# Kernel optimization log

Hardware: AMD Instinct MI355X
Metric: run time of the kernel (lower is better)

## Reference

```python
import jax, jax.numpy as jnp
import numpy as np

H = 12      # num_attention_heads
DM = 768    # hidden_size
HD = DM // H  # head_dim = 64


def setup_inputs() -> dict:
    key = jax.random.key(0)
    ks = jax.random.split(key, 9)
    B, L = 4, 2048
    s = 0.02
    return {
        "hidden_states": jax.random.normal(ks[0], (B, L, DM), jnp.float32),
        "wq": jax.random.normal(ks[1], (DM, DM), jnp.float32) * s,
        "bq": jnp.zeros((DM,), jnp.float32),
        "wk": jax.random.normal(ks[2], (DM, DM), jnp.float32) * s,
        "bk": jnp.zeros((DM,), jnp.float32),
        "wv": jax.random.normal(ks[3], (DM, DM), jnp.float32) * s,
        "bv": jnp.zeros((DM,), jnp.float32),
        "wo": jax.random.normal(ks[4], (DM, DM), jnp.float32) * s,
        "bo": jnp.zeros((DM,), jnp.float32),
    }


def reference(hidden_states, wq, bq, wk, bk, wv, bv, wo, bo):
    B, L, D = hidden_states.shape
    scale = HD ** -0.5
    # torch Linear: x @ W.T + b
    q = hidden_states @ wq.T + bq
    k = hidden_states @ wk.T + bk
    v = hidden_states @ wv.T + bv
    # [B, H, L, HD]
    q = q.reshape(B, L, H, HD).transpose(0, 2, 1, 3)
    k = k.reshape(B, L, H, HD).transpose(0, 2, 1, 3)
    v = v.reshape(B, L, H, HD).transpose(0, 2, 1, 3)
    attn = jnp.einsum('bhqd,bhkd->bhqk', q, k) * scale
    causal = jnp.tril(jnp.ones((L, L), dtype=bool))
    attn = jnp.where(causal, attn, jnp.float32(-jnp.inf))
    attn = jax.nn.softmax(attn, axis=-1)
    out = jnp.einsum('bhqk,bhkd->bhqd', attn, v)
    out = out.transpose(0, 2, 1, 3).reshape(B, L, D)
    return out @ wo.T + bo
```

## Files before the change

### kernel.cpp

```cpp
#include <hip/hip_runtime.h>

typedef unsigned short ushort_t;
typedef __attribute__((ext_vector_type(8))) short short8;
typedef __attribute__((ext_vector_type(4))) float f32x4;

__device__ __forceinline__ ushort_t f2b(float f) {
    union { float f; unsigned int i; } v; v.f = f;
    unsigned int x = v.i;
    return (ushort_t)((x + 0x7fffu + ((x >> 16) & 1u)) >> 16);
}
__device__ __forceinline__ ushort_t f2b_fast(float f) {
    union { float f; unsigned int i; } v; v.f = f;
    return (ushort_t)((v.i + 0x8000u) >> 16);
}
__device__ __forceinline__ float exp2_hw(float x) {
    return __builtin_amdgcn_exp2f(x);
}
__device__ __forceinline__ void dma16(const ushort_t* g, ushort_t* l) {
    __builtin_amdgcn_global_load_lds(
        (const __attribute__((address_space(1))) unsigned int*)g,
        (__attribute__((address_space(3))) unsigned int*)l, 16, 0, 0);
}

__global__ __launch_bounds__(256)
void convert_bf16(const float* __restrict__ hs, const float* __restrict__ wq,
                  const float* __restrict__ wk, const float* __restrict__ wv,
                  const float* __restrict__ wo,
                  ushort_t* __restrict__ hsb, ushort_t* __restrict__ wqb,
                  ushort_t* __restrict__ wkb, ushort_t* __restrict__ wvb,
                  ushort_t* __restrict__ wob)
{
    const int y = blockIdx.y;
    const float* src; ushort_t* dst; int n;
    if (y == 0)      { src = hs; dst = hsb; n = 8192 * 768; }
    else if (y == 1) { src = wq; dst = wqb; n = 768 * 768; }
    else if (y == 2) { src = wk; dst = wkb; n = 768 * 768; }
    else if (y == 3) { src = wv; dst = wvb; n = 768 * 768; }
    else             { src = wo; dst = wob; n = 768 * 768; }
    const int idx = (blockIdx.x * 256 + threadIdx.x) * 8;
    if (idx >= n) return;
    const float4 a = ((const float4*)(src + idx))[0];
    const float4 b = ((const float4*)(src + idx))[1];
    ushort_t tmp[8] = { f2b(a.x), f2b(a.y), f2b(a.z), f2b(a.w),
                        f2b(b.x), f2b(b.y), f2b(b.z), f2b(b.w) };
    *(uint4*)(dst + idx) = *(const uint4*)tmp;
}

#define AKG 130
#define NIT 24

template<int MODE>
__global__ __launch_bounds__(256, 3)
void gemm_mfma(const ushort_t* __restrict__ A,
               const ushort_t* __restrict__ W0, const ushort_t* __restrict__ W1,
               const ushort_t* __restrict__ W2,
               const float* __restrict__ b0, const float* __restrict__ b1,
               const float* __restrict__ b2,
               void* __restrict__ C0, void* __restrict__ C1, void* __restrict__ C2)
{
    __shared__ __attribute__((aligned(16))) ushort_t Ab[3][4 * AKG * 8];
    __shared__ __attribute__((aligned(16))) ushort_t Wb[3][4 * AKG * 8];

    const int id   = blockIdx.x;
    const int xcd  = id & 7;
    const int slot = id >> 3;
    int mtile, otile, z;
    if (MODE == 0) {
        mtile = (slot / 18) * 8 + xcd;
        const int rem = slot % 18;
        otile = rem % 6;
        z     = rem / 6;
    } else {
        mtile = (slot / 6) * 8 + xcd;
        otile = slot % 6;
        z     = 0;
    }
    const ushort_t* W = (z == 0) ? W0 : (z == 1) ? W1 : W2;
    const float* bias  = (z == 0) ? b0 : (z == 1) ? b1 : b2;
    void* C            = (z == 0) ? C0 : (z == 1) ? C1 : C2;

    const int t    = threadIdx.x;
    const int lane = t & 63;
    const int w    = t >> 6;
    const int col  = lane & 15;
    const int kg   = lane >> 4;
    const int m0   = mtile * 128;
    const int o0   = otile * 128;
    const int mh   = (w & 1) * 64;
    const int oh   = (w >> 1) * 64;

    f32x4 acc[4][4];
#pragma unroll
    for (int mt = 0; mt < 4; ++mt)
#pragma unroll
        for (int nt = 0; nt < 4; ++nt) acc[mt][nt] = (f32x4){0.f, 0.f, 0.f, 0.f};

    const ushort_t* pa = A + (size_t)(m0 + lane) * 768;
    const ushort_t* pw = W + (size_t)(o0 + lane) * 768;

#pragma unroll
    for (int c = 0; c < 2; ++c)
#pragma unroll
        for (int h = 0; h < 2; ++h) {
            dma16(pa + (size_t)h * 64 * 768 + c * 32 + w * 8,
                  &Ab[c][(w * AKG + h * 64) * 8]);
            dma16(pw + (size_t)h * 64 * 768 + c * 32 + w * 8,
                  &Wb[c][(w * AKG + h * 64) * 8]);
        }

    int cur = 0;
    for (int it = 0; it < NIT; ++it) {
        __builtin_amdgcn_s_barrier();
        __builtin_amdgcn_sched_barrier(0);

        if (it + 2 < NIT) {
            const int c   = it + 2;
            const int buf = (cur >= 1) ? cur - 1 : cur + 2;
#pragma unroll
            for (int h = 0; h < 2; ++h) {
                dma16(pa + (size_t)h * 64 * 768 + c * 32 + w * 8,
                      &Ab[buf][(w * AKG + h * 64) * 8]);
                dma16(pw + (size_t)h * 64 * 768 + c * 32 + w * 8,
                      &Wb[buf][(w * AKG + h * 64) * 8]);
            }
            asm volatile("s_waitcnt vmcnt(8)" ::: "memory");
        } else if (it + 1 < NIT) {
            asm volatile("s_waitcnt vmcnt(4)" ::: "memory");
        } else {
            asm volatile("s_waitcnt vmcnt(0)" ::: "memory");
        }
        __builtin_amdgcn_sched_barrier(0);

        short8 wf[4], af[4];
#pragma unroll
        for (int nt = 0; nt < 4; ++nt)
            wf[nt] = *(const short8*)&Wb[cur][(kg * AKG + oh + nt * 16 + col) * 8];
#pragma unroll
        for (int mt = 0; mt < 4; ++mt)
            af[mt] = *(const short8*)&Ab[cur][(kg * AKG + mh + mt * 16 + col) * 8];

#pragma unroll
        for (int mt = 0; mt < 4; ++mt)
#pragma unroll
            for (int nt = 0; nt < 4; ++nt)
                acc[mt][nt] = __builtin_amdgcn_mfma_f32_16x16x32_bf16(
                    af[mt], wf[nt], acc[mt][nt], 0, 0, 0);

        cur = (cur == 2) ? 0 : cur + 1;
    }

    float bias_v[4];
#pragma unroll
    for (int nt = 0; nt < 4; ++nt) bias_v[nt] = bias[o0 + oh + nt * 16 + col];
    const float scale = (MODE == 0 && z == 0) ? 0.18033688011112042f : 1.0f;

#pragma unroll
    for (int mt = 0; mt < 4; ++mt)
#pragma unroll
        for (int nt = 0; nt < 4; ++nt) {
            const int mb = m0 + mh + mt * 16 + kg * 4;
            const int o  = o0 + oh + nt * 16 + col;
            if (MODE == 0 && z == 2) {
                ushort_t tmp[4];
#pragma unroll
                for (int r = 0; r < 4; ++r) tmp[r] = f2b(acc[mt][nt][r] + bias_v[nt]);
                const size_t dst = ((size_t)((mb >> 11) * 12 + (o >> 6)) << 17)
                                 + ((size_t)(o & 63) << 11) + (mb & 2047);
                *(uint2*)((ushort_t*)C + dst) = *(const uint2*)tmp;
            } else {
#pragma unroll
                for (int r = 0; r < 4; ++r) {
                    const int m = mb + r;
                    const float v = (acc[mt][nt][r] + bias_v[nt]) * scale;
                    if (MODE == 0) {
                        const size_t dst = ((size_t)((m >> 11) * 12 + (o >> 6)) << 17)
                                         + ((size_t)(m & 2047) << 6) + (o & 63);
                        ((ushort_t*)C)[dst] = f2b(v);
                    } else {
                        ((float*)C)[(size_t)m * 768 + o] = v;
                    }
                }
            }
        }
}

#define KV_STRIDE 72
#define PS_STRIDE 76

__global__ __launch_bounds__(256, 3)
void attn_mfma(const ushort_t* __restrict__ Q, const ushort_t* __restrict__ K,
               const ushort_t* __restrict__ Vt, ushort_t* __restrict__ AO)
{
    __shared__ ushort_t Ks[64 * KV_STRIDE];
    __shared__ ushort_t Vs[64 * KV_STRIDE];
    __shared__ ushort_t Ps[4][16 * PS_STRIDE];

    const int t    = threadIdx.x;
    const int lane = t & 63;
    const int w    = t >> 6;
    const int id   = blockIdx.x;
    const int bh   = ((id >> 3) >> 4) * 8 + (id & 7);
    const int p    = (id >> 3) & 15;
    const size_t base = (size_t)bh << 17;

    const int col = lane & 15;
    const int kg  = lane >> 4;
    const int srow = t >> 2;
    const int scol = (t & 3) << 4;
    const int b = bh / 12, h = bh % 12;

#pragma unroll
    for (int phase = 0; phase < 2; ++phase) {
        const int tile = phase ? p : (31 - p);
        const int q0   = tile << 6;
        const int nch  = tile + 1;

        const ushort_t* pq = Q + base + (size_t)(q0 + 16 * w + col) * 64 + kg * 8;
        const short8 aq0 = *(const short8*)pq;
        const short8 aq1 = *(const short8*)(pq + 32);

        float l_lane[4] = {0.f, 0.f, 0.f, 0.f};
        f32x4 o_acc[4];
#pragma unroll
        for (int vt = 0; vt < 4; ++vt) o_acc[vt] = (f32x4){0.f, 0.f, 0.f, 0.f};

        uint4 ka, kb, va, vb;
        {
            const ushort_t* pk = K  + base + (size_t)srow * 64 + scol;
            const ushort_t* pv = Vt + base + ((size_t)srow << 11) + scol;
            ka = *(const uint4*)pk; kb = *(const uint4*)(pk + 8);
            va = *(const uint4*)pv; vb = *(const uint4*)(pv + 8);
        }

        for (int c = 0; c < nch; ++c) {
            __syncthreads();
            *(uint4*)&Ks[srow * KV_STRIDE + scol]     = ka;
            *(uint4*)&Ks[srow * KV_STRIDE + scol + 8] = kb;
            *(uint4*)&Vs[srow * KV_STRIDE + scol]     = va;
            *(uint4*)&Vs[srow * KV_STRIDE + scol + 8] = vb;
            __syncthreads();

            if (c + 1 < nch) {
                const int k1 = (c + 1) << 6;
                const ushort_t* pk = K  + base + (size_t)(k1 + srow) * 64 + scol;
                const ushort_t* pv = Vt + base + ((size_t)srow << 11) + k1 + scol;
                ka = *(const uint4*)pk; kb = *(const uint4*)(pk + 8);
                va = *(const uint4*)pv; vb = *(const uint4*)(pv + 8);
            }

            f32x4 s[4];
#pragma unroll
            for (int kt = 0; kt < 4; ++kt) {
                const ushort_t* pkf = &Ks[(kt * 16 + col) * KV_STRIDE + kg * 8];
                const short8 b0 = *(const short8*)pkf;
                const short8 b1 = *(const short8*)(pkf + 32);
                f32x4 acc = (f32x4){0.f, 0.f, 0.f, 0.f};
                acc = __builtin_amdgcn_mfma_f32_16x16x32_bf16(aq0, b0, acc, 0, 0, 0);
                acc = __builtin_amdgcn_mfma_f32_16x16x32_bf16(aq1, b1, acc, 0, 0, 0);
                s[kt] = acc;
            }

            const int qrow = q0 + 16 * w + 4 * kg;
            if (c == nch - 1) {
                const int k0 = c << 6;
#pragma unroll
                for (int kt = 0; kt < 4; ++kt)
#pragma unroll
                    for (int r = 0; r < 4; ++r) {
                        const int key = k0 + kt * 16 + col;
                        s[kt][r] = (key > qrow + r) ? 0.f : exp2_hw(s[kt][r]);
                    }
            } else {
#pragma unroll
                for (int kt = 0; kt < 4; ++kt)
#pragma unroll
                    for (int r = 0; r < 4; ++r) s[kt][r] = exp2_hw(s[kt][r]);
            }
#pragma unroll
            for (int r = 0; r < 4; ++r)
                l_lane[r] += (s[0][r] + s[1][r]) + (s[2][r] + s[3][r]);

            ushort_t* ps = Ps[w];
#pragma unroll
            for (int kt = 0; kt < 4; ++kt)
#pragma unroll
                for (int r = 0; r < 4; ++r)
                    ps[(4 * kg + r) * PS_STRIDE + kt * 16 + col] = f2b_fast(s[kt][r]);
            short8 pa0, pa1;
            {
                const ushort_t* pp = ps + (size_t)col * PS_STRIDE + kg * 8;
                pa0 = *(const short8*)pp;
                pa1 = *(const short8*)(pp + 32);
            }

#pragma unroll
            for (int vt = 0; vt < 4; ++vt) {
                const ushort_t* pvf = &Vs[(vt * 16 + col) * KV_STRIDE + kg * 8];
                const short8 v0 = *(const short8*)pvf;
                const short8 v1 = *(const short8*)(pvf + 32);
                f32x4 o = o_acc[vt];
                o = __builtin_amdgcn_mfma_f32_16x16x32_bf16(pa0, v0, o, 0, 0, 0);
                o = __builtin_amdgcn_mfma_f32_16x16x32_bf16(pa1, v1, o, 0, 0, 0);
                o_acc[vt] = o;
            }
        }

        float linv[4];
#pragma unroll
        for (int r = 0; r < 4; ++r) {
            float ls = l_lane[r];
            ls += __shfl_xor(ls, 1);
            ls += __shfl_xor(ls, 2);
            ls += __shfl_xor(ls, 4);
            ls += __shfl_xor(ls, 8);
            linv[r] = 1.f / ls;
        }
#pragma unroll
        for (int vt = 0; vt < 4; ++vt)
#pragma unroll
            for (int r = 0; r < 4; ++r) {
                const int q = q0 + 16 * w + 4 * kg + r;
                AO[((size_t)(b * 2048 + q)) * 768 + h * 64 + vt * 16 + col] =
                    f2b_fast(o_acc[vt][r] * linv[r]);
            }
    }
}

extern "C" void kernel_launch(void* const* d_in, const int* in_sizes, int n_in,
                              void* d_out, int out_size, void* d_ws, size_t ws_size,
                              hipStream_t stream) {
    const float* hs = (const float*)d_in[0];
    const float* wq = (const float*)d_in[1];
    const float* bq = (const float*)d_in[2];
    const float* wk = (const float*)d_in[3];
    const float* bk = (const float*)d_in[4];
    const float* wv = (const float*)d_in[5];
    const float* bv = (const float*)d_in[6];
    const float* wo = (const float*)d_in[7];
    const float* bo = (const float*)d_in[8];
    float* out = (float*)d_out;

    const size_t NB = (size_t)8192 * 768;
    const size_t WN = (size_t)768 * 768;
    ushort_t* hsb = (ushort_t*)d_ws;
    ushort_t* Qb  = hsb + NB;
    ushort_t* Kb  = Qb + NB;
    ushort_t* Vtb = Kb + NB;
    ushort_t* wqb = Vtb + NB;
    ushort_t* wkb = wqb + WN;
    ushort_t* wvb = wkb + WN;
    ushort_t* wob = wvb + WN;
    ushort_t* AO  = hsb;

    dim3 blk(256);
    convert_bf16<<<dim3(3072, 5), blk, 0, stream>>>(hs, wq, wk, wv, wo,
                                                    hsb, wqb, wkb, wvb, wob);
    gemm_mfma<0><<<dim3(1152), blk, 0, stream>>>(hsb, wqb, wkb, wvb,
                                                 bq, bk, bv, Qb, Kb, Vtb);
    attn_mfma<<<dim3(768), blk, 0, stream>>>(Qb, Kb, Vtb, AO);
    gemm_mfma<1><<<dim3(384), blk, 0, stream>>>(AO, wob, wob, wob,
                                                bo, bo, bo, out, out, out);
}
```

Before: 259.5 us.

## Swizzle GEMM LDS layout, unroll triple buffer, and raise MFMA priority in attention

The GEMM's LDS staging moves from a padded k-group-major layout to a row-major 128x32 tile with an XOR swizzle on the 8-element group index. This is meant to avoid bank conflicts without padding and to make each DMA cover contiguous 64-byte row segments. The main loop is unrolled by three so buffer indices become compile-time constants, and the runtime cur/buf arithmetic goes away. In attention, the P scratch stride is changed and s_setprio brackets the MFMA sections so waves prioritize matrix issue; the risk is scheduling interference and alignment effects from the odd stride.

```diff
diff --git a/kernel.cpp b/kernel.cpp
--- a/kernel.cpp
+++ b/kernel.cpp
@@ -46,7 +46,6 @@
     *(uint4*)(dst + idx) = *(const uint4*)tmp;
 }
 
-#define AKG 130
 #define NIT 24
 
 template<int MODE>
@@ -58,8 +57,8 @@
                const float* __restrict__ b2,
                void* __restrict__ C0, void* __restrict__ C1, void* __restrict__ C2)
 {
-    __shared__ __attribute__((aligned(16))) ushort_t Ab[3][4 * AKG * 8];
-    __shared__ __attribute__((aligned(16))) ushort_t Wb[3][4 * AKG * 8];
+    __shared__ __attribute__((aligned(16))) ushort_t Ab[3][128 * 32];
+    __shared__ __attribute__((aligned(16))) ushort_t Wb[3][128 * 32];
 
     const int id   = blockIdx.x;
     const int xcd  = id & 7;
@@ -95,34 +94,26 @@
 #pragma unroll
         for (int nt = 0; nt < 4; ++nt) acc[mt][nt] = (f32x4){0.f, 0.f, 0.f, 0.f};
 
-    const ushort_t* pa = A + (size_t)(m0 + lane) * 768;
-    const ushort_t* pw = W + (size_t)(o0 + lane) * 768;
-
-#pragma unroll
-    for (int c = 0; c < 2; ++c)
-#pragma unroll
-        for (int h = 0; h < 2; ++h) {
-            dma16(pa + (size_t)h * 64 * 768 + c * 32 + w * 8,
-                  &Ab[c][(w * AKG + h * 64) * 8]);
-            dma16(pw + (size_t)h * 64 * 768 + c * 32 + w * 8,
-                  &Wb[c][(w * AKG + h * 64) * 8]);
-        }
-
-    int cur = 0;
-    for (int it = 0; it < NIT; ++it) {
+    const int lrow = lane >> 2;
+    const int lgr  = (lane & 3) ^ ((lane >> 3) & 3);
+    const ushort_t* pa = A + (size_t)(m0 + lrow) * 768 + lgr * 8;
+    const ushort_t* pw = W + (size_t)(o0 + lrow) * 768 + lgr * 8;
+
+    auto stage = [&](int c, int b) {
+#pragma unroll
+        for (int j = 0; j < 2; ++j) {
+            const int q = 2 * w + j;
+            dma16(pa + (size_t)q * (16 * 768) + c * 32, &Ab[b][q * 512]);
+            dma16(pw + (size_t)q * (16 * 768) + c * 32, &Wb[b][q * 512]);
+        }
+    };
+
+    const int gq = (kg ^ ((col >> 1) & 3)) * 8;
+
+    auto step = [&](int it, int cur, int nb) {
         __builtin_amdgcn_s_barrier();
-        __builtin_amdgcn_sched_barrier(0);
-
         if (it + 2 < NIT) {
-            const int c   = it + 2;
-            const int buf = (cur >= 1) ? cur - 1 : cur + 2;
-#pragma unroll
-            for (int h = 0; h < 2; ++h) {
-                dma16(pa + (size_t)h * 64 * 768 + c * 32 + w * 8,
-                      &Ab[buf][(w * AKG + h * 64) * 8]);
-                dma16(pw + (size_t)h * 64 * 768 + c * 32 + w * 8,
-                      &Wb[buf][(w * AKG + h * 64) * 8]);
-            }
+            stage(it + 2, nb);
             asm volatile("s_waitcnt vmcnt(8)" ::: "memory");
         } else if (it + 1 < NIT) {
             asm volatile("s_waitcnt vmcnt(4)" ::: "memory");
@@ -134,10 +125,10 @@
         short8 wf[4], af[4];
 #pragma unroll
         for (int nt = 0; nt < 4; ++nt)
-            wf[nt] = *(const short8*)&Wb[cur][(kg * AKG + oh + nt * 16 + col) * 8];
+            wf[nt] = *(const short8*)&Wb[cur][(oh + nt * 16 + col) * 32 + gq];
 #pragma unroll
         for (int mt = 0; mt < 4; ++mt)
-            af[mt] = *(const short8*)&Ab[cur][(kg * AKG + mh + mt * 16 + col) * 8];
+            af[mt] = *(const short8*)&Ab[cur][(mh + mt * 16 + col) * 32 + gq];
 
 #pragma unroll
         for (int mt = 0; mt < 4; ++mt)
@@ -145,8 +136,14 @@
             for (int nt = 0; nt < 4; ++nt)
                 acc[mt][nt] = __builtin_amdgcn_mfma_f32_16x16x32_bf16(
                     af[mt], wf[nt], acc[mt][nt], 0, 0, 0);
-
-        cur = (cur == 2) ? 0 : cur + 1;
+    };
+
+    stage(0, 0);
+    stage(1, 1);
+    for (int j = 0; j < NIT; j += 3) {
+        step(j + 0, 0, 2);
+        step(j + 1, 1, 0);
+        step(j + 2, 2, 1);
     }
 
     float bias_v[4];
@@ -185,7 +182,7 @@
 }
 
 #define KV_STRIDE 72
-#define PS_STRIDE 76
+#define PS_STRIDE 78
 
 __global__ __launch_bounds__(256, 3)
 void attn_mfma(const ushort_t* __restrict__ Q, const ushort_t* __restrict__ K,
@@ -249,6 +246,7 @@
             }
 
             f32x4 s[4];
+            __builtin_amdgcn_s_setprio(1);
 #pragma unroll
             for (int kt = 0; kt < 4; ++kt) {
                 const ushort_t* pkf = &Ks[(kt * 16 + col) * KV_STRIDE + kg * 8];
@@ -259,6 +257,7 @@
                 acc = __builtin_amdgcn_mfma_f32_16x16x32_bf16(aq1, b1, acc, 0, 0, 0);
                 s[kt] = acc;
             }
+            __builtin_amdgcn_s_setprio(0);
 
             const int qrow = q0 + 16 * w + 4 * kg;
             if (c == nch - 1) {
@@ -293,6 +292,7 @@
                 pa1 = *(const short8*)(pp + 32);
             }
 
+            __builtin_amdgcn_s_setprio(1);
 #pragma unroll
             for (int vt = 0; vt < 4; ++vt) {
                 const ushort_t* pvf = &Vs[(vt * 16 + col) * KV_STRIDE + kg * 8];
@@ -303,6 +303,7 @@
                 o = __builtin_amdgcn_mfma_f32_16x16x32_bf16(pa1, v1, o, 0, 0, 0);
                 o_acc[vt] = o;
             }
+            __builtin_amdgcn_s_setprio(0);
         }
 
         float linv[4];
```

Result: faster. 227.6 us (-12.3%).
